# Optimization experiments

Measured on AMD Instinct MI355X. Metric: run time of the kernel, lower is better.

## Reference

```python
import jax, jax.numpy as jnp
import numpy as np

B, A, D, F, O, NB = 64, 1024, 5, 256, 256, 6  # batch, max_atoms, max_degree, ishape, oshape, bond feat dim


def setup_inputs() -> dict:
    key = jax.random.key(0)
    k1, k2, k3, k4 = jax.random.split(key, 4)
    atoms = jax.random.normal(k1, (B, A, F), dtype=jnp.float32)
    bonds = jax.random.normal(k2, (B, A, D, NB), dtype=jnp.float32)
    # -1 marks missing neighbor (degree padding); valid indices in [0, A)
    edges = jax.random.randint(k3, (B, A, D), -1, A)
    # xavier-normal-ish init for the 6 degree-specific weights, stacked [6, F+NB, O]
    scale = (2.0 / (F + NB + O)) ** 0.5
    degW = jax.random.normal(k4, (6, F + NB, O), dtype=jnp.float32) * scale
    b = jnp.full((1, O), 0.01, dtype=jnp.float32)
    return {"atoms": atoms, "bonds": bonds, "edges": edges, "degW": degW, "b": b}


def reference(atoms, bonds, edges, degW, b):
    # atoms: [B, A, F]; bonds: [B, A, D, NB]; edges: [B, A, D] int (-1 = pad)
    degrees = (edges != -1).sum(-1, keepdims=True)  # [B, A, 1]
    # pad a zero row at index 0 so edge -1 -> 0 gathers the mask value 0
    padded = jnp.pad(atoms, ((0, 0), (1, 0), (0, 0)))  # [B, A+1, F]
    neigh = jax.vmap(lambda p, e: p[e])(padded, edges + 1)  # [B, A, D, F]
    summed_atom = atoms + neigh.sum(axis=2)  # include_self=True
    feats = jnp.concatenate([summed_atom, bonds.sum(axis=2)], axis=-1)  # [B, A, F+NB]
    out = jnp.zeros((atoms.shape[0], atoms.shape[1], degW.shape[-1]), atoms.dtype)
    for d in range(6):  # fixed small structural loop over degree buckets
        mask = (degrees == d).astype(atoms.dtype)  # [B, A, 1]
        out = out + jax.nn.sigmoid(feats @ degW[d] + b) * mask
    return out
```

## Files before the change

kernel.cpp:

```cpp
#include <hip/hip_runtime.h>
#include <hip/hip_fp16.h>
#include <cstdint>

#define BATCH  64
#define NATOMS 1024
#define DEG    5
#define FIN    256
#define OOUT   256
#define NBF    6
#define KDIM   262
#define NKT    9
#define MROWS  (BATCH * NATOMS)
#define MT     32
#define AS     296

#define FRAG_SHORTS (16 * NKT * 64 * 8)
#define ATH_SHORTS  ((size_t)MROWS * FIN)

typedef __attribute__((ext_vector_type(8))) short bf16x8;
typedef __attribute__((ext_vector_type(4))) float f32x4;
typedef __attribute__((ext_vector_type(4))) unsigned short u16x4;

__device__ __forceinline__ unsigned short f2bf(float x) {
    unsigned u = __float_as_uint(x);
    u += 0x7fff + ((u >> 16) & 1);
    return (unsigned short)(u >> 16);
}
__device__ __forceinline__ float bf2f(unsigned short h) {
    return __uint_as_float(((unsigned)h) << 16);
}
__device__ __forceinline__ float sigmoidf_(float x) {
    return 1.f / (1.f + __expf(-x));
}
__device__ __forceinline__ unsigned short f2h(float x) {
    return __half_as_ushort(__float2half(x));
}
__device__ __forceinline__ float h2f(unsigned short u) {
    return __half2float(__ushort_as_half(u));
}

__global__ __launch_bounds__(256)
void convert_pre_kernel(const float* __restrict__ degW, unsigned short* __restrict__ Wsw,
                        const float* __restrict__ atoms, unsigned short* __restrict__ atomsH,
                        int nWblk)
{
    if (blockIdx.x < (unsigned)nWblk) {
        const int idx = blockIdx.x * 256 + threadIdx.x;
        if (idx >= 6 * 16 * NKT * 64) return;
        const int lane = idx & 63;
        int r = idx >> 6;
        const int t = r % NKT; r /= NKT;
        const int g = r & 15;
        const int d = r >> 4;
        const int col  = g * 16 + (lane & 15);
        const int k0   = t * 32 + (lane >> 4) * 8;
        const float* __restrict__ W = degW + (size_t)d * KDIM * OOUT;
        unsigned short* dst = Wsw + (size_t)idx * 8;
        #pragma unroll
        for (int j = 0; j < 8; ++j) {
            const int k = k0 + j;
            dst[j] = f2bf((k < KDIM) ? W[(size_t)k * OOUT + col] : 0.f);
        }
    } else {
        const int nblk = gridDim.x - nWblk;
        size_t i = (size_t)(blockIdx.x - nWblk) * 256 + threadIdx.x;
        const size_t stride = (size_t)nblk * 256;
        const size_t total = ATH_SHORTS / 4;
        const f32x4* __restrict__ src = (const f32x4*)atoms;
        u16x4* __restrict__ dst = (u16x4*)atomsH;
        for (; i < total; i += stride) {
            f32x4 v = __builtin_nontemporal_load(&src[i]);
            u16x4 h;
            h.x = f2h(v.x); h.y = f2h(v.y); h.z = f2h(v.z); h.w = f2h(v.w);
            __builtin_nontemporal_store(h, &dst[i]);
        }
    }
}

__global__ __launch_bounds__(256)
void convert_w_kernel(const float* __restrict__ degW, unsigned short* __restrict__ Wsw,
                      int all6)
{
    const int total = (all6 ? 6 : 1) * 16 * NKT * 64;
    const int idx = blockIdx.x * 256 + threadIdx.x;
    if (idx >= total) return;
    const int lane = idx & 63;
    int r = idx >> 6;
    const int t = r % NKT; r /= NKT;
    const int g = r & 15;
    const int d = r >> 4;
    const int srcd = all6 ? d : DEG;
    const int col  = g * 16 + (lane & 15);
    const int k0   = t * 32 + (lane >> 4) * 8;
    const float* __restrict__ W = degW + (size_t)srcd * KDIM * OOUT;
    unsigned short* dst = Wsw + (size_t)idx * 8;
    #pragma unroll
    for (int j = 0; j < 8; ++j) {
        const int k = k0 + j;
        dst[j] = f2bf((k < KDIM) ? W[(size_t)k * OOUT + col] : 0.f);
    }
}

template <int MODE>
__global__ __launch_bounds__(256, 4)
void nfp_fused_kernel(const float* __restrict__ atoms, const unsigned short* __restrict__ atomsH,
                      const float* __restrict__ bonds, const int* __restrict__ edges,
                      const unsigned short* __restrict__ Wsw, const float* __restrict__ degW,
                      const float* __restrict__ bias, float* __restrict__ out)
{
    constexpr bool FP16N = (MODE == 2);
    constexpr bool ALL6  = (MODE >= 1);

    __shared__ short Afeat[MT * AS];
    __shared__ int   edg[MT * DEG];
    __shared__ int   deg_lds[MT];
    __shared__ int   degmask;

    const int tid  = threadIdx.x;
    const int lane = tid & 63;
    const int wave = tid >> 6;

    const int bid   = blockIdx.x;
    const int xcd   = bid & 7;
    const int per   = bid >> 3;
    const int batch = (per >> 5) * 8 + xcd;
    const int blk   = per & 31;
    const int row0  = batch * NATOMS + blk * MT;

    if (tid == 0) degmask = 0;
    if (tid < MT * DEG) edg[tid] = edges[row0 * DEG + tid];
    __syncthreads();
    if (tid < MT) {
        int dc = 0;
        #pragma unroll
        for (int d = 0; d < DEG; ++d) dc += (edg[tid * DEG + d] != -1) ? 1 : 0;
        deg_lds[tid] = dc;
        atomicOr(&degmask, 1 << dc);
    }

    const float* __restrict__ abase = atoms + ((size_t)batch << 10) * FIN;
    const unsigned short* __restrict__ hbase =
        FP16N ? atomsH + ((size_t)batch << 10) * FIN : atomsH;
    const int selfrow = blk * MT;
    const int mw = wave * 8;

#define GATHER_CHUNK(MB, NR)                                                          \
    {                                                                                 \
        f32x4 self[NR]; int msk[NR];                                                  \
        u16x4 nh[NR][DEG]; f32x4 nv[NR][DEG];                                         \
        _Pragma("unroll")                                                             \
        for (int r = 0; r < NR; ++r) {                                                \
            const int m = (MB) + r;                                                   \
            msk[r] = 0;                                                               \
            self[r] = __builtin_nontemporal_load(                                     \
                (const f32x4*)&abase[(size_t)(selfrow + m) * FIN + lane * 4]);        \
            _Pragma("unroll")                                                         \
            for (int d = 0; d < DEG; ++d) {                                           \
                const int e = edg[m * DEG + d];                                       \
                msk[r] |= (e >= 0) ? (1 << d) : 0;                                    \
                const int ei = (e >= 0) ? e : 0;          \
                if constexpr (FP16N)                                                  \
                    nh[r][d] = *(const u16x4*)&hbase[(size_t)ei * FIN + lane * 4];    \
                else                                                                  \
                    nv[r][d] = *(const f32x4*)&abase[(size_t)ei * FIN + lane * 4];    \
            }                                                                         \
        }                                                                             \
        _Pragma("unroll")                                                             \
        for (int r = 0; r < NR; ++r) {                                                \
            const int m = (MB) + r;                                                   \
            f32x4 v = self[r];                                                        \
            _Pragma("unroll")                                                         \
            for (int d = 0; d < DEG; ++d) {                                           \
                const float fl = ((msk[r] >> d) & 1) ? 1.f : 0.f;                     \
                if constexpr (FP16N) {                                                \
                    v.x += fl * h2f(nh[r][d].x); v.y += fl * h2f(nh[r][d].y);         \
                    v.z += fl * h2f(nh[r][d].z); v.w += fl * h2f(nh[r][d].w);         \
                } else {                                                              \
                    v.x += fl * nv[r][d].x; v.y += fl * nv[r][d].y;                   \
                    v.z += fl * nv[r][d].z; v.w += fl * nv[r][d].w;                   \
                }                                                                     \
            }                                                                         \
            u16x4 us;                                                                 \
            us.x = f2bf(v.x); us.y = f2bf(v.y); us.z = f2bf(v.z); us.w = f2bf(v.w);   \
            *(u16x4*)&Afeat[m * AS + lane * 4] = us;                                  \
        }                                                                             \
    }

    GATHER_CHUNK(mw + 0, 3)
    GATHER_CHUNK(mw + 3, 3)
    GATHER_CHUNK(mw + 6, 2)
#undef GATHER_CHUNK

    {
        const int mz = mw + (lane >> 3), pz = lane & 7;
        u16x4 zz = {0, 0, 0, 0};
        *(u16x4*)&Afeat[mz * AS + FIN + pz * 4] = zz;
        if (lane < 48) {
            const int r  = lane / 6;
            const int kk = lane - r * 6;
            const int m  = mw + r;
            const float* __restrict__ bb = bonds + ((size_t)(row0 + m)) * (DEG * NBF) + kk;
            const float bv = bb[0] + bb[NBF] + bb[2 * NBF] + bb[3 * NBF] + bb[4 * NBF];
            Afeat[m * AS + FIN + kk] = f2bf(bv);
        }
    }

    const unsigned short* __restrict__ Wb5 =
        Wsw + (ALL6 ? (size_t)DEG * FRAG_SHORTS : (size_t)0);
    const int fr = lane & 15;
    const int q  = lane >> 4;
    const int wn = wave * 64;

    bf16x8 b0[4];
    #pragma unroll
    for (int j = 0; j < 4; ++j)
        b0[j] = *(const bf16x8*)&Wb5[((size_t)((wave * 4 + j) * NKT) * 64 + lane) * 8];

    __syncthreads();

    auto gemm_pass = [&](const unsigned short* __restrict__ Wb, bf16x8 (&bini)[4],
                         f32x4 (&a)[2][4]) {
        bf16x8 bcur[4], bnxt[4], acur[2], anxt[2];
        #pragma unroll
        for (int j = 0; j < 4; ++j) bcur[j] = bini[j];
        #pragma unroll
        for (int i = 0; i < 2; ++i)
            acur[i] = *(const bf16x8*)&Afeat[(i * 16 + fr) * AS + q * 8];
        #pragma unroll
        for (int t = 0; t < NKT; ++t) {
            if (t + 1 < NKT) {
                #pragma unroll
                for (int j = 0; j < 4; ++j)
                    bnxt[j] = *(const bf16x8*)&Wb[((size_t)((wave * 4 + j) * NKT + t + 1) * 64 + lane) * 8];
                #pragma unroll
                for (int i = 0; i < 2; ++i)
                    anxt[i] = *(const bf16x8*)&Afeat[(i * 16 + fr) * AS + (t + 1) * 32 + q * 8];
            }
            #pragma unroll
            for (int i = 0; i < 2; ++i)
                #pragma unroll
                for (int j = 0; j < 4; ++j)
                    a[i][j] = __builtin_amdgcn_mfma_f32_16x16x32_bf16(acur[i], bcur[j], a[i][j], 0, 0, 0);
            if (t + 1 < NKT) {
                #pragma unroll
                for (int j = 0; j < 4; ++j) bcur[j] = bnxt[j];
                #pragma unroll
                for (int i = 0; i < 2; ++i) acur[i] = anxt[i];
            }
        }
    };

    auto epilogue = [&](f32x4 (&a)[2][4], int want) {
        #pragma unroll
        for (int j = 0; j < 4; ++j) {
            const int gn = wn + j * 16 + fr;
            const float bj = bias[gn];
            #pragma unroll
            for (int i = 0; i < 2; ++i) {
                #pragma unroll
                for (int r = 0; r < 4; ++r) {
                    const int lm = i * 16 + q * 4 + r;
                    if (deg_lds[lm] == want)
                        __builtin_nontemporal_store(sigmoidf_(a[i][j][r] + bj),
                                                    &out[((size_t)row0 + lm) * OOUT + gn]);
                }
            }
        }
    };

    f32x4 acc[2][4];
    #pragma unroll
    for (int i = 0; i < 2; ++i)
        #pragma unroll
        for (int j = 0; j < 4; ++j)
            acc[i][j] = (f32x4){0.f, 0.f, 0.f, 0.f};

    gemm_pass(Wb5, b0, acc);
    epilogue(acc, DEG);

    int dmask = degmask & 0x1F;
    if (dmask == 0) return;

    if constexpr (ALL6) {
        while (dmask) {
            const int d = __ffs(dmask) - 1;
            dmask &= dmask - 1;
            const unsigned short* __restrict__ Wd = Wsw + (size_t)d * FRAG_SHORTS;
            bf16x8 bd[4];
            #pragma unroll
            for (int j = 0; j < 4; ++j)
                bd[j] = *(const bf16x8*)&Wd[((size_t)((wave * 4 + j) * NKT) * 64 + lane) * 8];
            f32x4 a2[2][4];
            #pragma unroll
            for (int i = 0; i < 2; ++i)
                #pragma unroll
                for (int j = 0; j < 4; ++j)
                    a2[i][j] = (f32x4){0.f, 0.f, 0.f, 0.f};
            gemm_pass(Wd, bd, a2);
            epilogue(a2, d);
        }
    } else {
        for (int m = 0; m < MT; ++m) {
            const int dg = deg_lds[m];
            if (dg == DEG) continue;
            const float* __restrict__ W = degW + (size_t)dg * KDIM * OOUT;
            float s0 = 0.f, s1 = 0.f, s2 = 0.f, s3 = 0.f;
            #pragma unroll 2
            for (int k = 0; k < 260; k += 4) {
                const float w0 = W[(size_t)(k + 0) * OOUT + tid];
                const float w1 = W[(size_t)(k + 1) * OOUT + tid];
                const float w2 = W[(size_t)(k + 2) * OOUT + tid];
                const float w3 = W[(size_t)(k + 3) * OOUT + tid];
                s0 += bf2f(Afeat[m * AS + k + 0]) * w0;
                s1 += bf2f(Afeat[m * AS + k + 1]) * w1;
                s2 += bf2f(Afeat[m * AS + k + 2]) * w2;
                s3 += bf2f(Afeat[m * AS + k + 3]) * w3;
            }
            s0 += bf2f(Afeat[m * AS + 260]) * W[(size_t)260 * OOUT + tid];
            s1 += bf2f(Afeat[m * AS + 261]) * W[(size_t)261 * OOUT + tid];
            const float x = ((s0 + s1) + (s2 + s3)) + bias[tid];
            out[((size_t)row0 + m) * OOUT + tid] = sigmoidf_(x);
        }
    }
}

#define FMT  32
#define FKT  32
#define FKPAD 288
__global__ __launch_bounds__(256, 2)
void nfp_conv_fallback(const float* __restrict__ atoms, const float* __restrict__ bonds,
                       const int* __restrict__ edges, const float* __restrict__ degW,
                       const float* __restrict__ bias, float* __restrict__ out)
{
    __shared__ float feats[FMT * FKPAD];
    __shared__ float wtile[FKT * OOUT];
    __shared__ int   edg[FMT * DEG];
    __shared__ int   deg_lds[FMT];
    __shared__ int   odd_list[FMT];
    __shared__ int   odd_cnt;
    __shared__ float b_lds[OOUT];

    const int tid = threadIdx.x, bid = blockIdx.x;
    const int batch = bid >> 5, a0 = (bid & 31) * FMT;
    const size_t atom_base = (size_t)batch * NATOMS;

    b_lds[tid] = bias[tid];
    if (tid == 0) odd_cnt = 0;
    if (tid < FMT * DEG) {
        const int m = tid / DEG, d = tid % DEG;
        edg[tid] = edges[(atom_base + a0 + m) * DEG + d];
    }
    __syncthreads();
    if (tid < FMT) {
        int dc = 0;
        #pragma unroll
        for (int d = 0; d < DEG; ++d) dc += (edg[tid * DEG + d] != -1) ? 1 : 0;
        deg_lds[tid] = dc;
        if (dc != DEG) { const int idx = atomicAdd(&odd_cnt, 1); odd_list[idx] = tid; }
    }
    __syncthreads();
    {
        const int f = tid;
        for (int m = 0; m < FMT; ++m) {
            float v = atoms[(atom_base + a0 + m) * FIN + f];
            #pragma unroll
            for (int d = 0; d < DEG; ++d) {
                const int e = edg[m * DEG + d];
                if (e >= 0) v += atoms[(atom_base + e) * FIN + f];
            }
            feats[m * FKPAD + f] = v;
        }
        #pragma unroll
        for (int t = 0; t < 4; ++t) {
            const int idx = t * 256 + tid;
            const int m = idx >> 5, kk = idx & 31;
            float v = 0.f;
            if (kk < NBF) {
                const size_t bb = (atom_base + a0 + m) * (size_t)(DEG * NBF);
                #pragma unroll
                for (int d = 0; d < DEG; ++d) v += bonds[bb + d * NBF + kk];
            }
            feats[m * FKPAD + FIN + kk] = v;
        }
    }
    const float* __restrict__ W5 = degW + (size_t)DEG * KDIM * OOUT;
    float acc[4][8];
    #pragma unroll
    for (int i = 0; i < 4; ++i)
        #pragma unroll
        for (int j = 0; j < 8; ++j) acc[i][j] = 0.f;
    const int tx = tid & 31, ty = tid >> 5;
    for (int kt = 0; kt < FKPAD; kt += FKT) {
        __syncthreads();
        #pragma unroll
        for (int t = 0; t < FKT; ++t) {
            const int k = kt + t;
            wtile[t * OOUT + tid] = (k < KDIM) ? W5[(size_t)k * OOUT + tid] : 0.f;
        }
        __syncthreads();
        #pragma unroll 4
        for (int r = 0; r < FKT; ++r) {
            float a_frag[4];
            #pragma unroll
            for (int i = 0; i < 4; ++i) a_frag[i] = feats[(ty * 4 + i) * FKPAD + kt + r];
            float w_frag[8];
            #pragma unroll
            for (int j = 0; j < 8; ++j) w_frag[j] = wtile[r * OOUT + tx + j * 32];
            #pragma unroll
            for (int i = 0; i < 4; ++i)
                #pragma unroll
                for (int j = 0; j < 8; ++j) acc[i][j] += a_frag[i] * w_frag[j];
        }
    }
    #pragma unroll
    for (int i = 0; i < 4; ++i) {
        const int m = ty * 4 + i;
        if (deg_lds[m] == DEG) {
            const size_t row = (atom_base + a0 + m) * (size_t)OOUT;
            #pragma unroll
            for (int j = 0; j < 8; ++j) {
                const int o = tx + j * 32;
                out[row + o] = sigmoidf_(acc[i][j] + b_lds[o]);
            }
        }
    }
    const int ocnt = odd_cnt;
    for (int i = 0; i < ocnt; ++i) {
        const int m = odd_list[i], d = deg_lds[m];
        const float* __restrict__ W = degW + (size_t)d * KDIM * OOUT;
        float a2 = 0.f;
        for (int k = 0; k < KDIM; ++k) a2 += feats[m * FKPAD + k] * W[(size_t)k * OOUT + tid];
        const size_t row = (atom_base + a0 + m) * (size_t)OOUT;
        out[row + tid] = sigmoidf_(a2 + b_lds[tid]);
    }
}

extern "C" void kernel_launch(void* const* d_in, const int* in_sizes, int n_in,
                              void* d_out, int out_size, void* d_ws, size_t ws_size,
                              hipStream_t stream) {
    const float* atoms = (const float*)d_in[0];
    const float* bonds = (const float*)d_in[1];
    const int*   edges = (const int*)d_in[2];
    const float* degW  = (const float*)d_in[3];
    const float* bias  = (const float*)d_in[4];
    float* out = (float*)d_out;

    const size_t WSW_ONE = (size_t)FRAG_SHORTS * 2;
    const size_t WSW_ALL = (size_t)6 * FRAG_SHORTS * 2;
    const size_t ATH_B   = ATH_SHORTS * 2;

    if (ws_size >= WSW_ALL + ATH_B) {
        unsigned short* Wsw    = (unsigned short*)d_ws;
        unsigned short* atomsH = (unsigned short*)((char*)d_ws + WSW_ALL);
        const int nWblk = (6 * 16 * NKT * 64 + 255) / 256;
        convert_pre_kernel<<<nWblk + 2048, 256, 0, stream>>>(degW, Wsw, atoms, atomsH, nWblk);
        nfp_fused_kernel<2><<<MROWS / MT, 256, 0, stream>>>(
            atoms, atomsH, bonds, edges, Wsw, degW, bias, out);
    } else if (ws_size >= WSW_ALL) {
        unsigned short* Wsw = (unsigned short*)d_ws;
        convert_w_kernel<<<(6 * 16 * NKT * 64 + 255) / 256, 256, 0, stream>>>(degW, Wsw, 1);
        nfp_fused_kernel<1><<<MROWS / MT, 256, 0, stream>>>(
            atoms, nullptr, bonds, edges, Wsw, degW, bias, out);
    } else if (ws_size >= WSW_ONE) {
        unsigned short* Wsw = (unsigned short*)d_ws;
        convert_w_kernel<<<(16 * NKT * 64 + 255) / 256, 256, 0, stream>>>(degW, Wsw, 0);
        nfp_fused_kernel<0><<<MROWS / MT, 256, 0, stream>>>(
            atoms, nullptr, bonds, edges, Wsw, degW, bias, out);
    } else {
        nfp_conv_fallback<<<BATCH * (NATOMS / FMT), 256, 0, stream>>>(
            atoms, bonds, edges, degW, bias, out);
    }
}
```

Before: 214.9 us.

## Split gather/feature build into prep kernel and run separate bf16 GEMM kernel

Replaces the fused gather+GEMM kernel with two kernels. A prep kernel converts the weights, gathers the neighbour sums, reduces the bond features, writes bf16 feature rows with padding to a workspace and stores a per-row degree byte. A new GEMM kernel with 64-row tiles copies those rows into LDS and runs the degree-bucketed MFMA passes. This decouples the latency-bound gather from the MFMA work and gives larger tiles, at the cost of an extra round trip of the feature matrix through global memory and a non-nontemporal output store.

```diff
diff --git a/kernel.cpp b/kernel.cpp
--- a/kernel.cpp
+++ b/kernel.cpp
@@ -16,6 +16,7 @@
 
 #define FRAG_SHORTS (16 * NKT * 64 * 8)
 #define ATH_SHORTS  ((size_t)MROWS * FIN)
+#define NWBLK 216
 
 typedef __attribute__((ext_vector_type(8))) short bf16x8;
 typedef __attribute__((ext_vector_type(4))) float f32x4;
@@ -38,6 +39,167 @@
 __device__ __forceinline__ float h2f(unsigned short u) {
     return __half2float(__ushort_as_half(u));
 }
+
+__global__ __launch_bounds__(256, 8)
+void prep_kernel(const float* __restrict__ degW, unsigned short* __restrict__ Wsw,
+                 const float* __restrict__ atoms, const float* __restrict__ bonds,
+                 const int* __restrict__ edges,
+                 unsigned short* __restrict__ feats, unsigned char* __restrict__ degB)
+{
+    if (blockIdx.x < NWBLK) {
+        const int idx = blockIdx.x * 256 + threadIdx.x;
+        const int lane = idx & 63;
+        int r = idx >> 6;
+        const int t = r % NKT; r /= NKT;
+        const int g = r & 15;
+        const int d = r >> 4;
+        const int col  = g * 16 + (lane & 15);
+        const int k0   = t * 32 + (lane >> 4) * 8;
+        const float* __restrict__ W = degW + (size_t)d * KDIM * OOUT;
+        unsigned short* dst = Wsw + (size_t)idx * 8;
+        #pragma unroll
+        for (int j = 0; j < 8; ++j) {
+            const int k = k0 + j;
+            dst[j] = f2bf((k < KDIM) ? W[(size_t)k * OOUT + col] : 0.f);
+        }
+        return;
+    }
+
+    const int wid  = ((blockIdx.x - NWBLK) * 256 + (int)threadIdx.x) >> 6;
+    const int lane = threadIdx.x & 63;
+    const int r0   = wid * 8;
+
+    int ev[8];
+    #pragma unroll
+    for (int rr = 0; rr < 8; ++rr)
+        ev[rr] = (lane < DEG) ? edges[(size_t)(r0 + rr) * DEG + lane] : -1;
+
+    for (int rr = 0; rr < 8; ++rr) {
+        const int row = r0 + rr;
+        const float* __restrict__ abase = atoms + ((size_t)(row >> 10) << 10) * FIN;
+        const int dg = (int)__popcll(__ballot(ev[rr] >= 0));
+
+        f32x4 v = *(const f32x4*)&atoms[(size_t)row * FIN + lane * 4];
+        #pragma unroll
+        for (int d = 0; d < DEG; ++d) {
+            const int ed = __shfl(ev[rr], d);
+            const f32x4 nv = *(const f32x4*)&abase[(size_t)((ed >= 0) ? ed : 0) * FIN + lane * 4];
+            const float fl = (ed >= 0) ? 1.f : 0.f;
+            v.x += fl * nv.x; v.y += fl * nv.y; v.z += fl * nv.z; v.w += fl * nv.w;
+        }
+        u16x4 us;
+        us.x = f2bf(v.x); us.y = f2bf(v.y); us.z = f2bf(v.z); us.w = f2bf(v.w);
+        *(u16x4*)&feats[(size_t)row * AS + lane * 4] = us;
+
+        float bx = (lane < DEG * NBF) ? bonds[(size_t)row * (DEG * NBF) + lane] : 0.f;
+        const int kk = (lane < NBF) ? lane : 0;
+        float bs = 0.f;
+        #pragma unroll
+        for (int p = 0; p < DEG; ++p) bs += __shfl(bx, kk + NBF * p);
+        if (lane < NBF)       feats[(size_t)row * AS + FIN + lane] = f2bf(bs);
+        else if (lane < 32)   feats[(size_t)row * AS + FIN + lane] = 0;
+        if (lane == 0)        degB[row] = (unsigned char)dg;
+    }
+}
+
+#define BM 64
+__global__ __launch_bounds__(256, 4)
+void nfp_gemm_kernel(const unsigned short* __restrict__ feats,
+                     const unsigned char* __restrict__ degB,
+                     const unsigned short* __restrict__ Wsw,
+                     const float* __restrict__ bias, float* __restrict__ out)
+{
+    __shared__ __align__(16) short At[BM * AS];
+    __shared__ int deg_lds[BM];
+    __shared__ int degmask;
+
+    const int tid  = threadIdx.x;
+    const int lane = tid & 63;
+    const int wave = tid >> 6;
+    const int row0 = blockIdx.x * BM;
+
+    if (tid == 0) degmask = 0;
+    __syncthreads();
+
+    if (tid < BM) {
+        const int dg = degB[row0 + tid];
+        deg_lds[tid] = dg;
+        atomicOr(&degmask, 1 << dg);
+    }
+    {
+        const bf16x8* __restrict__ src = (const bf16x8*)(feats + (size_t)row0 * AS);
+        bf16x8* dstv = (bf16x8*)At;
+        for (int off = tid; off < BM * AS / 8; off += 256)
+            dstv[off] = src[off];
+    }
+    __syncthreads();
+
+    const int fr = lane & 15;
+    const int q  = lane >> 4;
+    const int wn = wave * 64;
+
+    float bj[4];
+    #pragma unroll
+    for (int j = 0; j < 4; ++j) bj[j] = bias[wn + j * 16 + fr];
+
+    auto gemm_pass = [&](const unsigned short* __restrict__ Wb, f32x4 (&a)[4][4]) {
+        #pragma unroll
+        for (int t = 0; t < NKT; ++t) {
+            bf16x8 b[4], af[4];
+            #pragma unroll
+            for (int j = 0; j < 4; ++j)
+                b[j] = *(const bf16x8*)&Wb[((size_t)((wave * 4 + j) * NKT + t) * 64 + lane) * 8];
+            #pragma unroll
+            for (int i = 0; i < 4; ++i)
+                af[i] = *(const bf16x8*)&At[(i * 16 + fr) * AS + t * 32 + q * 8];
+            #pragma unroll
+            for (int i = 0; i < 4; ++i)
+                #pragma unroll
+                for (int j = 0; j < 4; ++j)
+                    a[i][j] = __builtin_amdgcn_mfma_f32_16x16x32_bf16(af[i], b[j], a[i][j], 0, 0, 0);
+        }
+    };
+    auto epilogue = [&](f32x4 (&a)[4][4], int want) {
+        #pragma unroll
+        for (int i = 0; i < 4; ++i) {
+            #pragma unroll
+            for (int r = 0; r < 4; ++r) {
+                const int lm = i * 16 + q * 4 + r;
+                if (deg_lds[lm] == want) {
+                    float* __restrict__ orow = out + (size_t)(row0 + lm) * OOUT + wn + fr;
+                    #pragma unroll
+                    for (int j = 0; j < 4; ++j)
+                        orow[j * 16] = sigmoidf_(a[i][j][r] + bj[j]);
+                }
+            }
+        }
+    };
+
+    f32x4 acc[4][4];
+    #pragma unroll
+    for (int i = 0; i < 4; ++i)
+        #pragma unroll
+        for (int j = 0; j < 4; ++j)
+            acc[i][j] = (f32x4){0.f, 0.f, 0.f, 0.f};
+
+    gemm_pass(Wsw + (size_t)DEG * FRAG_SHORTS, acc);
+    epilogue(acc, DEG);
+
+    int dmask = degmask & 0x1F;
+    while (dmask) {
+        const int d = __ffs(dmask) - 1;
+        dmask &= dmask - 1;
+        f32x4 a2[4][4];
+        #pragma unroll
+        for (int i = 0; i < 4; ++i)
+            #pragma unroll
+            for (int j = 0; j < 4; ++j)
+                a2[i][j] = (f32x4){0.f, 0.f, 0.f, 0.f};
+        gemm_pass(Wsw + (size_t)d * FRAG_SHORTS, a2);
+        epilogue(a2, d);
+    }
+}
+
 
 __global__ __launch_bounds__(256)
 void convert_pre_kernel(const float* __restrict__ degW, unsigned short* __restrict__ Wsw,
@@ -158,7 +320,7 @@
             for (int d = 0; d < DEG; ++d) {                                           \
                 const int e = edg[m * DEG + d];                                       \
                 msk[r] |= (e >= 0) ? (1 << d) : 0;                                    \
-                const int ei = (e >= 0) ? e : 0;          \
+                const int ei = (e >= 0) ? e : 0;                                      \
                 if constexpr (FP16N)                                                  \
                     nh[r][d] = *(const u16x4*)&hbase[(size_t)ei * FIN + lane * 4];    \
                 else                                                                  \
@@ -254,14 +416,14 @@
         #pragma unroll
         for (int j = 0; j < 4; ++j) {
             const int gn = wn + j * 16 + fr;
-            const float bj = bias[gn];
+            const float bjv = bias[gn];
             #pragma unroll
             for (int i = 0; i < 2; ++i) {
                 #pragma unroll
                 for (int r = 0; r < 4; ++r) {
                     const int lm = i * 16 + q * 4 + r;
                     if (deg_lds[lm] == want)
-                        __builtin_nontemporal_store(sigmoidf_(a[i][j][r] + bj),
+                        __builtin_nontemporal_store(sigmoidf_(a[i][j][r] + bjv),
                                                     &out[((size_t)row0 + lm) * OOUT + gn]);
                 }
             }
@@ -448,8 +610,17 @@
     const size_t WSW_ONE = (size_t)FRAG_SHORTS * 2;
     const size_t WSW_ALL = (size_t)6 * FRAG_SHORTS * 2;
     const size_t ATH_B   = ATH_SHORTS * 2;
-
-    if (ws_size >= WSW_ALL + ATH_B) {
+    const size_t FEATS_B = (size_t)MROWS * AS * 2;
+    const size_t NEED_SPLIT = WSW_ALL + FEATS_B + (size_t)MROWS;
+
+    if (ws_size >= NEED_SPLIT) {
+        unsigned short* Wsw   = (unsigned short*)d_ws;
+        unsigned short* feats = (unsigned short*)((char*)d_ws + WSW_ALL);
+        unsigned char*  degB  = (unsigned char*)((char*)d_ws + WSW_ALL + FEATS_B);
+        prep_kernel<<<NWBLK + MROWS / (4 * 8), 256, 0, stream>>>(
+            degW, Wsw, atoms, bonds, edges, feats, degB);
+        nfp_gemm_kernel<<<MROWS / BM, 256, 0, stream>>>(feats, degB, Wsw, bias, out);
+    } else if (ws_size >= WSW_ALL + ATH_B) {
         unsigned short* Wsw    = (unsigned short*)d_ws;
         unsigned short* atomsH = (unsigned short*)((char*)d_ws + WSW_ALL);
         const int nWblk = (6 * 16 * NKT * 64 + 255) / 256;
```

Result: slower. 250.9 us (+16.7%).
